# Kernel tuning notes

Measured on AMD Instinct MI355X. Metric: run time of the kernel, lower is better.

The kernel has to match this reference:

```python
import jax, jax.numpy as jnp
import numpy as np

N_MODEL = 32          # self.n_model
TEMP = 0.05           # softmax temperature
LARGE_NEG = -float(np.log(1e10))


def setup_inputs() -> dict:
    key = jax.random.key(0)
    ks = jax.random.split(key, 20)
    B, D, N, seq_len, d_model, pred_len, in_dim = 4, 32, 768, 96, 128, 24, 3
    L = 2 * seq_len
    w = lambda k, shape: jax.random.normal(k, shape, jnp.float32) * 0.02
    return {
        "x_t": jax.random.normal(ks[0], (B, N, 16), jnp.float32),   # unused by forward
        "x": jax.random.normal(ks[1], (B, D, N, L), jnp.float32),
        "csta": jax.random.uniform(ks[2], (N, 2), jnp.float32),
        "cpan": jax.random.uniform(ks[3], (B, N, 2), jnp.float32),
        # Time_Attention Q/K/V: Linear(2*seq_len, d_model)
        "Wq": w(ks[4], (d_model, L)), "bq": jnp.zeros((d_model,), jnp.float32),
        "Wk": w(ks[5], (d_model, L)), "bk": jnp.zeros((d_model,), jnp.float32),
        "Wv": w(ks[6], (d_model, L)), "bv": jnp.zeros((d_model,), jnp.float32),
        # geo-graph embeddings
        "W_sta": w(ks[7], (N_MODEL, 2)), "b_sta": jnp.zeros((N_MODEL,), jnp.float32),
        "W_n1": w(ks[8], (N_MODEL, 3 * N_MODEL)), "b_n1": jnp.zeros((N_MODEL,), jnp.float32),
        "W_n2": w(ks[9], (N_MODEL, 3 * N_MODEL)), "b_n2": jnp.zeros((N_MODEL,), jnp.float32),
        "distance_scale": jnp.asarray(2.0, jnp.float32),
        # output heads: fc1 Linear(d_model, pred_len), fc2 Linear(2*d_mark=32, in_dim)
        "W_fc1": w(ks[10], (pred_len, d_model)), "b_fc1": jnp.zeros((pred_len,), jnp.float32),
        "W_fc2": w(ks[11], (in_dim, 2 * 16)), "b_fc2": jnp.zeros((in_dim,), jnp.float32),
    }


def _l2norm(v, axis=1, eps=1e-12):
    n = jnp.sqrt(jnp.sum(v * v, axis=axis, keepdims=True))
    return v / jnp.maximum(n, eps)


def _geo_graph(csta_n, W_sta, b_sta, W_n1, b_n1, W_n2, b_n2, distance_scale):
    nodevec = csta_n @ W_sta.T + b_sta                      # [N, 32]
    node_c = jnp.concatenate([jnp.sin(nodevec), jnp.cos(nodevec), nodevec], axis=1)  # [N, 96]
    nv1 = _l2norm(jax.nn.relu(node_c @ W_n1.T + b_n1))
    nv2 = _l2norm(jax.nn.relu(node_c @ W_n2.T + b_n2))
    geo_sim = nv1 @ nv2.T                                   # [N, N]
    lat, lon = csta_n[:, 0], csta_n[:, 1]
    dist = jnp.sqrt((lat[:, None] - lat[None, :]) ** 2 + (lon[:, None] - lon[None, :]) ** 2 + 1e-8)
    dscale = jax.nn.sigmoid(distance_scale) * 3.0
    dist_sim = jnp.exp(-dist * dscale)
    combined = geo_sim * 0.6 + dist_sim * 0.4 + 0.05
    return (combined + combined.T) / 2.0


def reference(x_t, x, csta, cpan, Wq, bq, Wk, bk, Wv, bv,
              W_sta, b_sta, W_n1, b_n1, W_n2, b_n2, distance_scale,
              W_fc1, b_fc1, W_fc2, b_fc2):
    B, D, N, L = x.shape
    pred_len, d_model = W_fc1.shape
    in_dim = W_fc2.shape[0]

    # robust min-max normalization of station coordinates
    lat_v, lon_v = cpan[:, :, 0], cpan[:, :, 1]
    rng = jnp.stack([lat_v.max() - lat_v.min() + 1e-8, lon_v.max() - lon_v.min() + 1e-8])
    mins = jnp.stack([lat_v.min(), lon_v.min()])
    csta_n = (csta - mins) / rng                            # [N, 2]

    geo_graph = _geo_graph(csta_n, W_sta, b_sta, W_n1, b_n1, W_n2, b_n2, distance_scale)

    # Time_Attention over fused batch-channel axis
    xr = x.reshape(B * D, N, L)
    q = xr @ Wq.T + bq                                      # [BD, N, d]
    k = xr @ Wk.T + bk
    v = xr @ Wv.T + bv
    scale = 1.0 / np.sqrt(d_model)
    scores = jnp.einsum('bnd,bmd->bnm', q, k) * scale       # [BD, N, N]
    add_mask = jnp.where(geo_graph == 0, LARGE_NEG, 0.0)
    scores = scores * geo_graph[None] + add_mask[None]
    A = jax.nn.softmax(scores / TEMP, axis=-1)              # dropout = identity (eval)
    t = jnp.einsum('bnm,bmd->bnd', A, v)                    # [BD, N, d]

    out = t @ W_fc1.T + b_fc1                               # [BD, N, pred_len]
    out = out.reshape(B, D, N, pred_len).transpose(0, 3, 2, 1).reshape(-1, N, D)
    out = out @ W_fc2.T + b_fc2                             # [B*P, N, in_dim]
    out = out.reshape(B, pred_len, N, in_dim).transpose(0, 3, 2, 1)  # [B, in_dim, N, pred_len]
    return out, A, geo_graph
```

## Files before the change

kernel.cpp:

```cpp
#include <hip/hip_runtime.h>
#include <math.h>

#define NN 768
#define DM 128
#define LL 192
#define BD 128
#define OUT_OFF_A   221184
#define OUT_OFF_GEO 75718656

#define WS_CN   16
#define WS_NV1  2048
#define WS_NV2  26624
#define WS_GEOS 51200
#define WS_WH   641024
#define WS_W1H  677888
#define WS_QH   739328
#define WS_KH   7030784
#define WS_VT   13322240
#define WS_O1   19613696

constexpr float TEMP_INV    = 20.0f;
constexpr float QK_SCALE    = 0.08838834764831845f;
constexpr float LOG2E       = 1.4426950408889634f;
constexpr float GS_SCALE    = QK_SCALE * TEMP_INV * LOG2E;

typedef unsigned short u16;
typedef u16 u16x8 __attribute__((ext_vector_type(8)));
typedef u16 u16x4 __attribute__((ext_vector_type(4)));
typedef __bf16 bf16x8 __attribute__((ext_vector_type(8)));
typedef float f32x4 __attribute__((ext_vector_type(4)));

__device__ __forceinline__ u16 f2b(float f) {
  unsigned u = __builtin_bit_cast(unsigned, f);
  return (u16)((u + 0x7fffu + ((u >> 16) & 1u)) >> 16);
}

__device__ __forceinline__ void lds_barrier() {
  asm volatile("s_waitcnt lgkmcnt(0)" ::: "memory");
  __builtin_amdgcn_s_barrier();
}

__global__ __launch_bounds__(256) void k_prep(const float* __restrict__ cpan,
                                              const float* __restrict__ csta,
                                              float* __restrict__ ws) {
  __shared__ float red[4][4];
  int t = threadIdx.x;
  float mnla = 1e30f, mxla = -1e30f, mnlo = 1e30f, mxlo = -1e30f;
  for (int i = t; i < 3072; i += 256) {
    float la = cpan[i * 2 + 0], lo = cpan[i * 2 + 1];
    mnla = fminf(mnla, la); mxla = fmaxf(mxla, la);
    mnlo = fminf(mnlo, lo); mxlo = fmaxf(mxlo, lo);
  }
  for (int off = 1; off < 64; off <<= 1) {
    mnla = fminf(mnla, __shfl_xor(mnla, off));
    mxla = fmaxf(mxla, __shfl_xor(mxla, off));
    mnlo = fminf(mnlo, __shfl_xor(mnlo, off));
    mxlo = fmaxf(mxlo, __shfl_xor(mxlo, off));
  }
  if ((t & 63) == 0) {
    int w = t >> 6;
    red[0][w] = mnla; red[1][w] = mxla; red[2][w] = mnlo; red[3][w] = mxlo;
  }
  __syncthreads();
  mnla = fminf(fminf(red[0][0], red[0][1]), fminf(red[0][2], red[0][3]));
  mxla = fmaxf(fmaxf(red[1][0], red[1][1]), fmaxf(red[1][2], red[1][3]));
  mnlo = fminf(fminf(red[2][0], red[2][1]), fminf(red[2][2], red[2][3]));
  mxlo = fmaxf(fmaxf(red[3][0], red[3][1]), fmaxf(red[3][2], red[3][3]));
  float rla = mxla - mnla + 1e-8f;
  float rlo = mxlo - mnlo + 1e-8f;
  float* cn = ws + WS_CN;
  for (int i = t; i < NN; i += 256) {
    cn[i * 2 + 0] = (csta[i * 2 + 0] - mnla) / rla;
    cn[i * 2 + 1] = (csta[i * 2 + 1] - mnlo) / rlo;
  }
}

__global__ __launch_bounds__(256) void k_cvtw(const float* __restrict__ Wq, const float* __restrict__ Wk,
                                              const float* __restrict__ Wv, const float* __restrict__ W_fc1,
                                              u16* __restrict__ wh, u16* __restrict__ w1h) {
  int i = (blockIdx.x * 256 + threadIdx.x) * 4;
  if (i < 73728) {
    const float* src = (i < 24576) ? (Wq + i) : ((i < 49152) ? (Wk + i - 24576) : (Wv + i - 49152));
    float4 v = *(const float4*)src;
    u16x4 o = {f2b(v.x), f2b(v.y), f2b(v.z), f2b(v.w)};
    *(u16x4*)(wh + i) = o;
  } else {
    int j = i - 73728;
    if (j < 4096) {
      int row = j >> 7;
      u16x4 o = {0, 0, 0, 0};
      if (row < 24) {
        float4 v = *(const float4*)(W_fc1 + (size_t)row * 128 + (j & 127));
        o.x = f2b(v.x); o.y = f2b(v.y); o.z = f2b(v.z); o.w = f2b(v.w);
      }
      *(u16x4*)(w1h + j) = o;
    }
  }
}

__global__ __launch_bounds__(64) void k_nodes(const float* __restrict__ cn,
                                              const float* __restrict__ W_sta, const float* __restrict__ b_sta,
                                              const float* __restrict__ W_n1, const float* __restrict__ b_n1,
                                              const float* __restrict__ W_n2, const float* __restrict__ b_n2,
                                              float* __restrict__ nv1, float* __restrict__ nv2) {
  __shared__ float node_c[96];
  int i = blockIdx.x, t = threadIdx.x;
  float c0 = cn[i * 2 + 0], c1 = cn[i * 2 + 1];
  if (t < 32) {
    float nv = c0 * W_sta[t * 2 + 0] + c1 * W_sta[t * 2 + 1] + b_sta[t];
    node_c[t] = sinf(nv);
    node_c[32 + t] = cosf(nv);
    node_c[64 + t] = nv;
  }
  __syncthreads();
  int half = t >> 5, o = t & 31;
  const float* W = half ? W_n2 : W_n1;
  const float* b = half ? b_n2 : b_n1;
  float acc = b[o];
  for (int j = 0; j < 96; ++j) acc = fmaf(node_c[j], W[o * 96 + j], acc);
  acc = fmaxf(acc, 0.0f);
  float ss = acc * acc;
  for (int off = 1; off < 32; off <<= 1) ss += __shfl_xor(ss, off);
  float nrm = fmaxf(sqrtf(ss), 1e-12f);
  (half ? nv2 : nv1)[i * 32 + o] = acc / nrm;
}

__global__ __launch_bounds__(256) void k_geo(const float* __restrict__ nv1, const float* __restrict__ nv2,
                                             const float* __restrict__ cn, const float* __restrict__ dsc_in,
                                             float* __restrict__ geo, float* __restrict__ geoS) {
  int idx = blockIdx.x * 256 + threadIdx.x;
  if (idx >= NN * NN) return;
  int i = idx / NN, j = idx % NN;
  float d1 = 0.f, d2 = 0.f;
  for (int o = 0; o < 32; ++o) {
    d1 = fmaf(nv1[i * 32 + o], nv2[j * 32 + o], d1);
    d2 = fmaf(nv1[j * 32 + o], nv2[i * 32 + o], d2);
  }
  float dla = cn[i * 2] - cn[j * 2], dlo = cn[i * 2 + 1] - cn[j * 2 + 1];
  float dist = sqrtf(dla * dla + dlo * dlo + 1e-8f);
  float x = dsc_in[0];
  float dscale = (1.0f / (1.0f + expf(-x))) * 3.0f;
  float dsim = expf(-dist * dscale);
  float g = 0.3f * (d1 + d2) + 0.4f * dsim + 0.05f;
  geo[idx] = g;
  geoS[idx] = g * GS_SCALE;
}

__global__ __launch_bounds__(256) void k_qkv(const float* __restrict__ x, const u16* __restrict__ wh,
      const float* __restrict__ bq, const float* __restrict__ bk, const float* __restrict__ bv,
      u16* __restrict__ qo, u16* __restrict__ ko, u16* __restrict__ vTo) {
  int z = blockIdx.y;
  const u16* W = wh + z * 24576;
  const float* bias = (z == 0) ? bq : ((z == 1) ? bk : bv);
  __shared__ u16 xs[128 * 192];
  int m0 = blockIdx.x * 128;
  int t = threadIdx.x;
  const float* xg = x + (size_t)m0 * 192;
  for (int i = t; i < 3072; i += 256) {
    int row = i / 24, c = i % 24;
    float4 f0 = *(const float4*)(xg + (size_t)row * 192 + c * 8);
    float4 f1 = *(const float4*)(xg + (size_t)row * 192 + c * 8 + 4);
    u16x8 v8 = {f2b(f0.x), f2b(f0.y), f2b(f0.z), f2b(f0.w),
                f2b(f1.x), f2b(f1.y), f2b(f1.z), f2b(f1.w)};
    int byte = (row * 384 + c * 16) ^ ((row & 7) << 4);
    *(u16x8*)((char*)xs + byte) = v8;
  }
  __syncthreads();
  int w = t >> 6, l = t & 63, wr = w >> 1, wc = w & 1, lg = l >> 4, lm = l & 15;
  f32x4 acc[4][4] = {};
#pragma unroll
  for (int kk = 0; kk < 6; ++kk) {
    bf16x8 a[4], b[4];
#pragma unroll
    for (int fr = 0; fr < 4; ++fr) {
      int row = wr * 64 + fr * 16 + lm;
      int byte = (row * 384 + kk * 64 + lg * 16) ^ ((row & 7) << 4);
      a[fr] = __builtin_bit_cast(bf16x8, *(const u16x8*)((const char*)xs + byte));
    }
#pragma unroll
    for (int fc = 0; fc < 4; ++fc) {
      int row = wc * 64 + fc * 16 + lm;
      b[fc] = __builtin_bit_cast(bf16x8, *(const u16x8*)(W + row * 192 + kk * 32 + lg * 8));
    }
#pragma unroll
    for (int fr = 0; fr < 4; ++fr)
#pragma unroll
      for (int fc = 0; fc < 4; ++fc)
        acc[fr][fc] = __builtin_amdgcn_mfma_f32_16x16x32_bf16(a[fr], b[fc], acc[fr][fc], 0, 0, 0);
  }
  if (z < 2) {
    u16* out = (z == 0) ? qo : ko;
#pragma unroll
    for (int fr = 0; fr < 4; ++fr)
#pragma unroll
      for (int fc = 0; fc < 4; ++fc) {
        int col = wc * 64 + fc * 16 + lm;
        float bb = bias[col];
#pragma unroll
        for (int r = 0; r < 4; ++r) {
          int row = m0 + wr * 64 + fr * 16 + lg * 4 + r;
          out[(size_t)row * 128 + col] = f2b(acc[fr][fc][r] + bb);
        }
      }
  } else {
    u16* es = xs;
    __syncthreads();
#pragma unroll
    for (int fr = 0; fr < 4; ++fr)
#pragma unroll
      for (int fc = 0; fc < 4; ++fc) {
        int col = wc * 64 + fc * 16 + lm;
        float bb = bias[col];
#pragma unroll
        for (int r = 0; r < 4; ++r) {
          int row = wr * 64 + fr * 16 + lg * 4 + r;
          es[row * 132 + col] = f2b(acc[fr][fc][r] + bb);
        }
      }
    __syncthreads();
    int col = t >> 1, half = t & 1;
    int bd = m0 / NN, ml = m0 % NN;
    u16* dst = vTo + (size_t)bd * 98304 + (size_t)col * NN + ml + half * 64;
#pragma unroll
    for (int i = 0; i < 64; i += 8) {
      u16x8 v8;
#pragma unroll
      for (int j = 0; j < 8; ++j) v8[j] = es[(half * 64 + i + j) * 132 + col];
      *(u16x8*)(dst + i) = v8;
    }
  }
}

__global__ __launch_bounds__(256, 4) void k_attn(const u16* __restrict__ qh, const u16* __restrict__ kh,
                                                 const u16* __restrict__ vT, const float* __restrict__ geoS,
                                                 const u16* __restrict__ w1h, const float* __restrict__ b_fc1,
                                                 float* __restrict__ Aout, float* __restrict__ o1) {
  int bd = blockIdx.x;
  int m0 = blockIdx.y * 64;
  __shared__ u16 ks[2][32 * 128];
  __shared__ u16 vs[2][128 * 32];
  __shared__ u16 pb[4][16 * 32];
  int t = threadIdx.x, w = t >> 6, l = t & 63, lm = l & 15, hi = l >> 4;
  const u16* qg = qh + ((size_t)bd * NN + m0) * 128;
  const u16* kg = kh + (size_t)bd * 98304;
  const u16* vg = vT + (size_t)bd * 98304;
  float* Ab = Aout + (size_t)bd * 589824 + (size_t)m0 * NN;
  const float* gb = geoS + (size_t)m0 * NN;

  bf16x8 qf[4];
#pragma unroll
  for (int kk = 0; kk < 4; ++kk)
    qf[kk] = __builtin_bit_cast(bf16x8,
        *(const u16x8*)(qg + (size_t)(w * 16 + lm) * 128 + kk * 32 + hi * 8));

#pragma unroll
  for (int i = 0; i < 2; ++i) {
    int idx = i * 256 + t, row = idx >> 4, cc = idx & 15;
    u16x8 v8 = *(const u16x8*)(kg + (size_t)row * 128 + cc * 8);
    int byte = (row * 256 + cc * 16) ^ ((row & 7) << 4);
    *(u16x8*)((char*)ks[0] + byte) = v8;
  }
  float gcur[2][4];
#pragma unroll
  for (int fc = 0; fc < 2; ++fc)
#pragma unroll
    for (int r = 0; r < 4; ++r)
      gcur[fc][r] = gb[(size_t)(w * 16 + hi * 4 + r) * NN + fc * 16 + lm];
  lds_barrier();
  float psum[4] = {0.f, 0.f, 0.f, 0.f};
  for (int c = 0; c < 24; ++c) {
    u16x8 kpre[2];
    float gnxt[2][4];
    if (c < 23) {
#pragma unroll
      for (int i = 0; i < 2; ++i) {
        int idx = i * 256 + t, row = idx >> 4, cc = idx & 15;
        kpre[i] = *(const u16x8*)(kg + (size_t)((c + 1) * 32 + row) * 128 + cc * 8);
      }
#pragma unroll
      for (int fc = 0; fc < 2; ++fc)
#pragma unroll
        for (int r = 0; r < 4; ++r)
          gnxt[fc][r] = gb[(size_t)(w * 16 + hi * 4 + r) * NN + (c + 1) * 32 + fc * 16 + lm];
    }
    const u16* kb = ks[c & 1];
    f32x4 acc[2] = {};
#pragma unroll
    for (int kk = 0; kk < 4; ++kk)
#pragma unroll
      for (int fc = 0; fc < 2; ++fc) {
        int row = fc * 16 + lm;
        int byte = (row * 256 + kk * 64 + hi * 16) ^ ((row & 7) << 4);
        bf16x8 b = __builtin_bit_cast(bf16x8, *(const u16x8*)((const char*)kb + byte));
        acc[fc] = __builtin_amdgcn_mfma_f32_16x16x32_bf16(qf[kk], b, acc[fc], 0, 0, 0);
      }
    if (c < 23) {
#pragma unroll
      for (int i = 0; i < 2; ++i) {
        int idx = i * 256 + t, row = idx >> 4, cc = idx & 15;
        int byte = (row * 256 + cc * 16) ^ ((row & 7) << 4);
        *(u16x8*)((char*)ks[(c + 1) & 1] + byte) = kpre[i];
      }
    }
#pragma unroll
    for (int fc = 0; fc < 2; ++fc)
#pragma unroll
      for (int r = 0; r < 4; ++r)
        psum[r] += __builtin_amdgcn_exp2f(fminf(acc[fc][r] * gcur[fc][r], 120.0f));
    if (c < 23) {
#pragma unroll
      for (int fc = 0; fc < 2; ++fc)
#pragma unroll
        for (int r = 0; r < 4; ++r) gcur[fc][r] = gnxt[fc][r];
    }
    lds_barrier();
  }
#pragma unroll
  for (int off = 1; off < 16; off <<= 1)
#pragma unroll
    for (int r = 0; r < 4; ++r) psum[r] += __shfl_xor(psum[r], off);
  float inv[4];
#pragma unroll
  for (int r = 0; r < 4; ++r) inv[r] = 1.0f / psum[r];

#pragma unroll
  for (int i = 0; i < 2; ++i) {
    int idx = i * 256 + t;
    int krow = idx >> 4, kcc = idx & 15;
    u16x8 kv8 = *(const u16x8*)(kg + (size_t)krow * 128 + kcc * 8);
    int kbyte = (krow * 256 + kcc * 16) ^ ((krow & 7) << 4);
    *(u16x8*)((char*)ks[0] + kbyte) = kv8;
    int vrow = idx >> 2, vcc = idx & 3;
    u16x8 vv8 = *(const u16x8*)(vg + (size_t)vrow * NN + vcc * 8);
    int vbyte = (vrow * 64 + vcc * 16) ^ ((vrow & 7) << 4);
    *(u16x8*)((char*)vs[0] + vbyte) = vv8;
  }
#pragma unroll
  for (int fc = 0; fc < 2; ++fc)
#pragma unroll
    for (int r = 0; r < 4; ++r)
      gcur[fc][r] = gb[(size_t)(w * 16 + hi * 4 + r) * NN + fc * 16 + lm];
  lds_barrier();
  f32x4 tacc[8] = {};
  u16* pw = pb[w];
  for (int c = 0; c < 24; ++c) {
    u16x8 kpre[2], vpre[2];
    float gnxt[2][4];
    if (c < 23) {
#pragma unroll
      for (int i = 0; i < 2; ++i) {
        int idx = i * 256 + t;
        int krow = idx >> 4, kcc = idx & 15;
        kpre[i] = *(const u16x8*)(kg + (size_t)((c + 1) * 32 + krow) * 128 + kcc * 8);
        int vrow = idx >> 2, vcc = idx & 3;
        vpre[i] = *(const u16x8*)(vg + (size_t)vrow * NN + (c + 1) * 32 + vcc * 8);
      }
#pragma unroll
      for (int fc = 0; fc < 2; ++fc)
#pragma unroll
        for (int r = 0; r < 4; ++r)
          gnxt[fc][r] = gb[(size_t)(w * 16 + hi * 4 + r) * NN + (c + 1) * 32 + fc * 16 + lm];
    }
    const u16* kb = ks[c & 1];
    f32x4 acc[2] = {};
#pragma unroll
    for (int kk = 0; kk < 4; ++kk)
#pragma unroll
      for (int fc = 0; fc < 2; ++fc) {
        int row = fc * 16 + lm;
        int byte = (row * 256 + kk * 64 + hi * 16) ^ ((row & 7) << 4);
        bf16x8 b = __builtin_bit_cast(bf16x8, *(const u16x8*)((const char*)kb + byte));
        acc[fc] = __builtin_amdgcn_mfma_f32_16x16x32_bf16(qf[kk], b, acc[fc], 0, 0, 0);
      }
    if (c < 23) {
#pragma unroll
      for (int i = 0; i < 2; ++i) {
        int idx = i * 256 + t;
        int krow = idx >> 4, kcc = idx & 15;
        int kbyte = (krow * 256 + kcc * 16) ^ ((krow & 7) << 4);
        *(u16x8*)((char*)ks[(c + 1) & 1] + kbyte) = kpre[i];
        int vrow = idx >> 2, vcc = idx & 3;
        int vbyte = (vrow * 64 + vcc * 16) ^ ((vrow & 7) << 4);
        *(u16x8*)((char*)vs[(c + 1) & 1] + vbyte) = vpre[i];
      }
    }
#pragma unroll
    for (int fc = 0; fc < 2; ++fc) {
      int col = c * 32 + fc * 16 + lm;
#pragma unroll
      for (int r = 0; r < 4; ++r) {
        int rl = w * 16 + hi * 4 + r;
        float u = __builtin_amdgcn_exp2f(fminf(acc[fc][r] * gcur[fc][r], 120.0f));
        float p = u * inv[r];
        __builtin_nontemporal_store(p, Ab + (size_t)rl * NN + col);
        int rloc = hi * 4 + r;
        int byte = (rloc * 64 + (fc * 16 + lm) * 2) ^ ((rloc & 7) << 4);
        *(u16*)((char*)pw + byte) = f2b(p);
      }
    }
    if (c < 23) {
#pragma unroll
      for (int fc = 0; fc < 2; ++fc)
#pragma unroll
        for (int r = 0; r < 4; ++r) gcur[fc][r] = gnxt[fc][r];
    }
    bf16x8 pa;
    {
      int byte = (lm * 64 + hi * 16) ^ ((lm & 7) << 4);
      pa = __builtin_bit_cast(bf16x8, *(const u16x8*)((const char*)pw + byte));
    }
    const u16* vb = vs[c & 1];
#pragma unroll
    for (int fc = 0; fc < 8; ++fc) {
      int row = fc * 16 + lm;
      int byte = (row * 64 + hi * 16) ^ ((row & 7) << 4);
      bf16x8 b = __builtin_bit_cast(bf16x8, *(const u16x8*)((const char*)vb + byte));
      tacc[fc] = __builtin_amdgcn_mfma_f32_16x16x32_bf16(pa, b, tacc[fc], 0, 0, 0);
    }
    lds_barrier();
  }

  u16* ts = (u16*)ks + w * 2048;
#pragma unroll
  for (int fc = 0; fc < 8; ++fc)
#pragma unroll
    for (int r = 0; r < 4; ++r) {
      int row = hi * 4 + r, col = fc * 16 + lm;
      int byte = (row * 256 + col * 2) ^ ((row & 7) << 4);
      *(u16*)((char*)ts + byte) = f2b(tacc[fc][r]);
    }
  f32x4 of[2] = {};
#pragma unroll
  for (int kk = 0; kk < 4; ++kk) {
    int byte = (lm * 256 + kk * 64 + hi * 16) ^ ((lm & 7) << 4);
    bf16x8 tf = __builtin_bit_cast(bf16x8, *(const u16x8*)((const char*)ts + byte));
#pragma unroll
    for (int g = 0; g < 2; ++g) {
      bf16x8 wf = __builtin_bit_cast(bf16x8,
          *(const u16x8*)(w1h + (size_t)(g * 16 + lm) * 128 + kk * 32 + hi * 8));
      of[g] = __builtin_amdgcn_mfma_f32_16x16x32_bf16(tf, wf, of[g], 0, 0, 0);
    }
  }
  int bi = bd >> 5, di = bd & 31;
#pragma unroll
  for (int g = 0; g < 2; ++g) {
    int pp = g * 16 + lm;
    if (pp < 24) {
      float bb = b_fc1[pp];
#pragma unroll
      for (int r = 0; r < 4; ++r) {
        int n = m0 + w * 16 + hi * 4 + r;
        __builtin_nontemporal_store(of[g][r] + bb,
            o1 + ((size_t)(bi * NN + n) * 32 + di) * 24 + pp);
      }
    }
  }
}

__global__ __launch_bounds__(256) void k_final2(const float* __restrict__ o1, const float* __restrict__ W_fc2,
                                                const float* __restrict__ b_fc2, float* __restrict__ out) {
  __shared__ float ol[2][768];
  __shared__ float w2[96];
  int t = threadIdx.x, half = t >> 7, tl = t & 127;
  int b = blockIdx.x / 384, np = blockIdx.x % 384;
  int n = np * 2 + half;
  const float* src = o1 + (size_t)(b * NN + n) * 768;
  if (t < 96) w2[t] = W_fc2[t];
  for (int i = tl; i < 192; i += 128)
    *(float4*)&ol[half][i * 4] = *(const float4*)(src + i * 4);
  __syncthreads();
  if (tl < 72) {
    int c = tl / 24, pp = tl % 24;
    float acc = b_fc2[c];
#pragma unroll
    for (int d = 0; d < 32; ++d) acc = fmaf(w2[c * 32 + d], ol[half][d * 24 + pp], acc);
    out[(((size_t)b * 3 + c) * NN + n) * 24 + pp] = acc;
  }
}

extern "C" void kernel_launch(void* const* d_in, const int* in_sizes, int n_in,
                              void* d_out, int out_size, void* d_ws, size_t ws_size,
                              hipStream_t stream) {
  (void)in_sizes; (void)n_in; (void)out_size; (void)ws_size;
  const float* x     = (const float*)d_in[1];
  const float* csta  = (const float*)d_in[2];
  const float* cpan  = (const float*)d_in[3];
  const float* Wq    = (const float*)d_in[4];
  const float* bq    = (const float*)d_in[5];
  const float* Wk    = (const float*)d_in[6];
  const float* bk    = (const float*)d_in[7];
  const float* Wv    = (const float*)d_in[8];
  const float* bv    = (const float*)d_in[9];
  const float* W_sta = (const float*)d_in[10];
  const float* b_sta = (const float*)d_in[11];
  const float* W_n1  = (const float*)d_in[12];
  const float* b_n1  = (const float*)d_in[13];
  const float* W_n2  = (const float*)d_in[14];
  const float* b_n2  = (const float*)d_in[15];
  const float* dsc   = (const float*)d_in[16];
  const float* W_fc1 = (const float*)d_in[17];
  const float* b_fc1 = (const float*)d_in[18];
  const float* W_fc2 = (const float*)d_in[19];
  const float* b_fc2 = (const float*)d_in[20];

  float* out  = (float*)d_out;
  float* Aout = out + OUT_OFF_A;
  float* geo  = out + OUT_OFF_GEO;

  float* ws   = (float*)d_ws;
  float* cn   = ws + WS_CN;
  float* nv1  = ws + WS_NV1;
  float* nv2  = ws + WS_NV2;
  float* geoS = ws + WS_GEOS;
  u16*   wh   = (u16*)(ws + WS_WH);
  u16*   w1h  = (u16*)(ws + WS_W1H);
  u16*   qh   = (u16*)(ws + WS_QH);
  u16*   kh   = (u16*)(ws + WS_KH);
  u16*   vT   = (u16*)(ws + WS_VT);
  float* o1   = ws + WS_O1;

  k_prep<<<1, 256, 0, stream>>>(cpan, csta, ws);
  k_cvtw<<<76, 256, 0, stream>>>(Wq, Wk, Wv, W_fc1, wh, w1h);
  k_nodes<<<768, 64, 0, stream>>>(cn, W_sta, b_sta, W_n1, b_n1, W_n2, b_n2, nv1, nv2);
  k_geo<<<(NN * NN + 255) / 256, 256, 0, stream>>>(nv1, nv2, cn, dsc, geo, geoS);

  k_qkv<<<dim3(768, 3), 256, 0, stream>>>(x, wh, bq, bk, bv, qh, kh, vT);
  k_attn<<<dim3(BD, 12), 256, 0, stream>>>(qh, kh, vT, geoS, w1h, b_fc1, Aout, o1);
  k_final2<<<1536, 256, 0, stream>>>(o1, W_fc2, b_fc2, out);
}
```

Before: 269.8 us.

## Fuse QKV projections per block and widen attention pass-one K tiles

The QKV kernel now stages each x tile into shared memory once and computes all three projections (Q, K, V) in a single block, rather than launching three blocks per tile that each reload and convert x. In the attention kernel, the first softmax-normalisation pass now processes 64-key chunks over 12 iterations instead of 32-key chunks over 24, using a unified shared buffer that is re-partitioned for the second pass. This cuts redundant x reads and conversions and halves the barrier count in pass one, at the cost of fewer QKV blocks for parallelism and more registers for the larger accumulators and prefetch arrays.

After: 280.4 us. 3.9% more time.

```diff
diff --git a/kernel.cpp b/kernel.cpp
--- a/kernel.cpp
+++ b/kernel.cpp
@@ -149,9 +149,6 @@
 __global__ __launch_bounds__(256) void k_qkv(const float* __restrict__ x, const u16* __restrict__ wh,
       const float* __restrict__ bq, const float* __restrict__ bk, const float* __restrict__ bv,
       u16* __restrict__ qo, u16* __restrict__ ko, u16* __restrict__ vTo) {
-  int z = blockIdx.y;
-  const u16* W = wh + z * 24576;
-  const float* bias = (z == 0) ? bq : ((z == 1) ? bk : bv);
   __shared__ u16 xs[128 * 192];
   int m0 = blockIdx.x * 128;
   int t = threadIdx.x;
@@ -167,29 +164,35 @@
   }
   __syncthreads();
   int w = t >> 6, l = t & 63, wr = w >> 1, wc = w & 1, lg = l >> 4, lm = l & 15;
-  f32x4 acc[4][4] = {};
-#pragma unroll
-  for (int kk = 0; kk < 6; ++kk) {
-    bf16x8 a[4], b[4];
-#pragma unroll
-    for (int fr = 0; fr < 4; ++fr) {
-      int row = wr * 64 + fr * 16 + lm;
-      int byte = (row * 384 + kk * 64 + lg * 16) ^ ((row & 7) << 4);
-      a[fr] = __builtin_bit_cast(bf16x8, *(const u16x8*)((const char*)xs + byte));
-    }
-#pragma unroll
-    for (int fc = 0; fc < 4; ++fc) {
-      int row = wc * 64 + fc * 16 + lm;
-      b[fc] = __builtin_bit_cast(bf16x8, *(const u16x8*)(W + row * 192 + kk * 32 + lg * 8));
-    }
-#pragma unroll
-    for (int fr = 0; fr < 4; ++fr)
-#pragma unroll
-      for (int fc = 0; fc < 4; ++fc)
-        acc[fr][fc] = __builtin_amdgcn_mfma_f32_16x16x32_bf16(a[fr], b[fc], acc[fr][fc], 0, 0, 0);
-  }
-  if (z < 2) {
-    u16* out = (z == 0) ? qo : ko;
+
+  auto compute = [&](const u16* W, f32x4 (&acc)[4][4]) {
+#pragma unroll
+    for (int kk = 0; kk < 6; ++kk) {
+      bf16x8 a[4], b[4];
+#pragma unroll
+      for (int fr = 0; fr < 4; ++fr) {
+        int row = wr * 64 + fr * 16 + lm;
+        int byte = (row * 384 + kk * 64 + lg * 16) ^ ((row & 7) << 4);
+        a[fr] = __builtin_bit_cast(bf16x8, *(const u16x8*)((const char*)xs + byte));
+      }
+#pragma unroll
+      for (int fc = 0; fc < 4; ++fc) {
+        int row = wc * 64 + fc * 16 + lm;
+        b[fc] = __builtin_bit_cast(bf16x8, *(const u16x8*)(W + row * 192 + kk * 32 + lg * 8));
+      }
+#pragma unroll
+      for (int fr = 0; fr < 4; ++fr)
+#pragma unroll
+        for (int fc = 0; fc < 4; ++fc)
+          acc[fr][fc] = __builtin_amdgcn_mfma_f32_16x16x32_bf16(a[fr], b[fc], acc[fr][fc], 0, 0, 0);
+    }
+  };
+
+  for (int z = 0; z < 2; ++z) {
+    f32x4 acc[4][4] = {};
+    compute(wh + z * 24576, acc);
+    const float* bias = z == 0 ? bq : bk;
+    u16* out = z == 0 ? qo : ko;
 #pragma unroll
     for (int fr = 0; fr < 4; ++fr)
 #pragma unroll
@@ -202,7 +205,10 @@
           out[(size_t)row * 128 + col] = f2b(acc[fr][fc][r] + bb);
         }
       }
-  } else {
+  }
+  {
+    f32x4 acc[4][4] = {};
+    compute(wh + 2 * 24576, acc);
     u16* es = xs;
     __syncthreads();
 #pragma unroll
@@ -210,7 +216,7 @@
 #pragma unroll
       for (int fc = 0; fc < 4; ++fc) {
         int col = wc * 64 + fc * 16 + lm;
-        float bb = bias[col];
+        float bb = bv[col];
 #pragma unroll
         for (int r = 0; r < 4; ++r) {
           int row = wr * 64 + fr * 16 + lg * 4 + r;
@@ -237,8 +243,7 @@
                                                  float* __restrict__ Aout, float* __restrict__ o1) {
   int bd = blockIdx.x;
   int m0 = blockIdx.y * 64;
-  __shared__ u16 ks[2][32 * 128];
-  __shared__ u16 vs[2][128 * 32];
+  __shared__ u16 smem[16384];
   __shared__ u16 pb[4][16 * 32];
   int t = threadIdx.x, w = t >> 6, l = t & 63, lm = l & 15, hi = l >> 4;
   const u16* qg = qh + ((size_t)bd * NN + m0) * 128;
@@ -254,62 +259,63 @@
         *(const u16x8*)(qg + (size_t)(w * 16 + lm) * 128 + kk * 32 + hi * 8));
 
 #pragma unroll
-  for (int i = 0; i < 2; ++i) {
+  for (int i = 0; i < 4; ++i) {
     int idx = i * 256 + t, row = idx >> 4, cc = idx & 15;
     u16x8 v8 = *(const u16x8*)(kg + (size_t)row * 128 + cc * 8);
     int byte = (row * 256 + cc * 16) ^ ((row & 7) << 4);
-    *(u16x8*)((char*)ks[0] + byte) = v8;
-  }
-  float gcur[2][4];
-#pragma unroll
-  for (int fc = 0; fc < 2; ++fc)
+    *(u16x8*)((char*)smem + byte) = v8;
+  }
+  float gcur[4][4];
+#pragma unroll
+  for (int fc = 0; fc < 4; ++fc)
 #pragma unroll
     for (int r = 0; r < 4; ++r)
       gcur[fc][r] = gb[(size_t)(w * 16 + hi * 4 + r) * NN + fc * 16 + lm];
   lds_barrier();
   float psum[4] = {0.f, 0.f, 0.f, 0.f};
-  for (int c = 0; c < 24; ++c) {
-    u16x8 kpre[2];
-    float gnxt[2][4];
-    if (c < 23) {
-#pragma unroll
-      for (int i = 0; i < 2; ++i) {
+  for (int c = 0; c < 12; ++c) {
+    int cbuf = (c & 1) * 16384;
+    int nbuf = 16384 - cbuf;
+    u16x8 kpre[4];
+    float gnxt[4][4];
+    if (c < 11) {
+#pragma unroll
+      for (int i = 0; i < 4; ++i) {
         int idx = i * 256 + t, row = idx >> 4, cc = idx & 15;
-        kpre[i] = *(const u16x8*)(kg + (size_t)((c + 1) * 32 + row) * 128 + cc * 8);
-      }
-#pragma unroll
-      for (int fc = 0; fc < 2; ++fc)
+        kpre[i] = *(const u16x8*)(kg + (size_t)((c + 1) * 64 + row) * 128 + cc * 8);
+      }
+#pragma unroll
+      for (int fc = 0; fc < 4; ++fc)
 #pragma unroll
         for (int r = 0; r < 4; ++r)
-          gnxt[fc][r] = gb[(size_t)(w * 16 + hi * 4 + r) * NN + (c + 1) * 32 + fc * 16 + lm];
-    }
-    const u16* kb = ks[c & 1];
-    f32x4 acc[2] = {};
+          gnxt[fc][r] = gb[(size_t)(w * 16 + hi * 4 + r) * NN + (c + 1) * 64 + fc * 16 + lm];
+    }
+    f32x4 acc[4] = {};
 #pragma unroll
     for (int kk = 0; kk < 4; ++kk)
 #pragma unroll
-      for (int fc = 0; fc < 2; ++fc) {
+      for (int fc = 0; fc < 4; ++fc) {
         int row = fc * 16 + lm;
-        int byte = (row * 256 + kk * 64 + hi * 16) ^ ((row & 7) << 4);
-        bf16x8 b = __builtin_bit_cast(bf16x8, *(const u16x8*)((const char*)kb + byte));
+        int byte = cbuf + ((row * 256 + kk * 64 + hi * 16) ^ ((row & 7) << 4));
+        bf16x8 b = __builtin_bit_cast(bf16x8, *(const u16x8*)((const char*)smem + byte));
         acc[fc] = __builtin_amdgcn_mfma_f32_16x16x32_bf16(qf[kk], b, acc[fc], 0, 0, 0);
       }
-    if (c < 23) {
-#pragma unroll
-      for (int i = 0; i < 2; ++i) {
+    if (c < 11) {
+#pragma unroll
+      for (int i = 0; i < 4; ++i) {
         int idx = i * 256 + t, row = idx >> 4, cc = idx & 15;
-        int byte = (row * 256 + cc * 16) ^ ((row & 7) << 4);
-        *(u16x8*)((char*)ks[(c + 1) & 1] + byte) = kpre[i];
-      }
-    }
-#pragma unroll
-    for (int fc = 0; fc < 2; ++fc)
+        int byte = nbuf + ((row * 256 + cc * 16) ^ ((row & 7) << 4));
+        *(u16x8*)((char*)smem + byte) = kpre[i];
+      }
+    }
+#pragma unroll
+    for (int fc = 0; fc < 4; ++fc)
 #pragma unroll
       for (int r = 0; r < 4; ++r)
         psum[r] += __builtin_amdgcn_exp2f(fminf(acc[fc][r] * gcur[fc][r], 120.0f));
-    if (c < 23) {
-#pragma unroll
-      for (int fc = 0; fc < 2; ++fc)
+    if (c < 11) {
+#pragma unroll
+      for (int fc = 0; fc < 4; ++fc)
 #pragma unroll
         for (int r = 0; r < 4; ++r) gcur[fc][r] = gnxt[fc][r];
     }
@@ -329,21 +335,26 @@
     int krow = idx >> 4, kcc = idx & 15;
     u16x8 kv8 = *(const u16x8*)(kg + (size_t)krow * 128 + kcc * 8);
     int kbyte = (krow * 256 + kcc * 16) ^ ((krow & 7) << 4);
-    *(u16x8*)((char*)ks[0] + kbyte) = kv8;
+    *(u16x8*)((char*)smem + kbyte) = kv8;
     int vrow = idx >> 2, vcc = idx & 3;
     u16x8 vv8 = *(const u16x8*)(vg + (size_t)vrow * NN + vcc * 8);
-    int vbyte = (vrow * 64 + vcc * 16) ^ ((vrow & 7) << 4);
-    *(u16x8*)((char*)vs[0] + vbyte) = vv8;
-  }
+    int vbyte = 16384 + ((vrow * 64 + vcc * 16) ^ ((vrow & 7) << 4));
+    *(u16x8*)((char*)smem + vbyte) = vv8;
+  }
+  float g2[2][4];
 #pragma unroll
   for (int fc = 0; fc < 2; ++fc)
 #pragma unroll
     for (int r = 0; r < 4; ++r)
-      gcur[fc][r] = gb[(size_t)(w * 16 + hi * 4 + r) * NN + fc * 16 + lm];
+      g2[fc][r] = gb[(size_t)(w * 16 + hi * 4 + r) * NN + fc * 16 + lm];
   lds_barrier();
   f32x4 tacc[8] = {};
   u16* pw = pb[w];
   for (int c = 0; c < 24; ++c) {
+    int kcur = (c & 1) * 8192;
+    int knxt = 8192 - kcur;
+    int vcur = 16384 + (c & 1) * 8192;
+    int vnxt = 16384 + (8192 - (vcur - 16384));
     u16x8 kpre[2], vpre[2];
     float gnxt[2][4];
     if (c < 23) {
@@ -361,15 +372,14 @@
         for (int r = 0; r < 4; ++r)
           gnxt[fc][r] = gb[(size_t)(w * 16 + hi * 4 + r) * NN + (c + 1) * 32 + fc * 16 + lm];
     }
-    const u16* kb = ks[c & 1];
     f32x4 acc[2] = {};
 #pragma unroll
     for (int kk = 0; kk < 4; ++kk)
 #pragma unroll
       for (int fc = 0; fc < 2; ++fc) {
         int row = fc * 16 + lm;
-        int byte = (row * 256 + kk * 64 + hi * 16) ^ ((row & 7) << 4);
-        bf16x8 b = __builtin_bit_cast(bf16x8, *(const u16x8*)((const char*)kb + byte));
+        int byte = kcur + ((row * 256 + kk * 64 + hi * 16) ^ ((row & 7) << 4));
+        bf16x8 b = __builtin_bit_cast(bf16x8, *(const u16x8*)((const char*)smem + byte));
         acc[fc] = __builtin_amdgcn_mfma_f32_16x16x32_bf16(qf[kk], b, acc[fc], 0, 0, 0);
       }
     if (c < 23) {
@@ -377,11 +387,11 @@
       for (int i = 0; i < 2; ++i) {
         int idx = i * 256 + t;
         int krow = idx >> 4, kcc = idx & 15;
-        int kbyte = (krow * 256 + kcc * 16) ^ ((krow & 7) << 4);
-        *(u16x8*)((char*)ks[(c + 1) & 1] + kbyte) = kpre[i];
+        int kbyte = knxt + ((krow * 256 + kcc * 16) ^ ((krow & 7) << 4));
+        *(u16x8*)((char*)smem + kbyte) = kpre[i];
         int vrow = idx >> 2, vcc = idx & 3;
-        int vbyte = (vrow * 64 + vcc * 16) ^ ((vrow & 7) << 4);
-        *(u16x8*)((char*)vs[(c + 1) & 1] + vbyte) = vpre[i];
+        int vbyte = vnxt + ((vrow * 64 + vcc * 16) ^ ((vrow & 7) << 4));
+        *(u16x8*)((char*)smem + vbyte) = vpre[i];
       }
     }
 #pragma unroll
@@ -390,7 +400,7 @@
 #pragma unroll
       for (int r = 0; r < 4; ++r) {
         int rl = w * 16 + hi * 4 + r;
-        float u = __builtin_amdgcn_exp2f(fminf(acc[fc][r] * gcur[fc][r], 120.0f));
+        float u = __builtin_amdgcn_exp2f(fminf(acc[fc][r] * g2[fc][r], 120.0f));
         float p = u * inv[r];
         __builtin_nontemporal_store(p, Ab + (size_t)rl * NN + col);
         int rloc = hi * 4 + r;
@@ -402,38 +412,37 @@
 #pragma unroll
       for (int fc = 0; fc < 2; ++fc)
 #pragma unroll
-        for (int r = 0; r < 4; ++r) gcur[fc][r] = gnxt[fc][r];
+        for (int r = 0; r < 4; ++r) g2[fc][r] = gnxt[fc][r];
     }
     bf16x8 pa;
     {
       int byte = (lm * 64 + hi * 16) ^ ((lm & 7) << 4);
       pa = __builtin_bit_cast(bf16x8, *(const u16x8*)((const char*)pw + byte));
     }
-    const u16* vb = vs[c & 1];
 #pragma unroll
     for (int fc = 0; fc < 8; ++fc) {
       int row = fc * 16 + lm;
-      int byte = (row * 64 + hi * 16) ^ ((row & 7) << 4);
-      bf16x8 b = __builtin_bit_cast(bf16x8, *(const u16x8*)((const char*)vb + byte));
+      int byte = vcur + ((row * 64 + hi * 16) ^ ((row & 7) << 4));
+      bf16x8 b = __builtin_bit_cast(bf16x8, *(const u16x8*)((const char*)smem + byte));
       tacc[fc] = __builtin_amdgcn_mfma_f32_16x16x32_bf16(pa, b, tacc[fc], 0, 0, 0);
     }
     lds_barrier();
   }
 
-  u16* ts = (u16*)ks + w * 2048;
+  char* ts = (char*)smem + w * 4096;
 #pragma unroll
   for (int fc = 0; fc < 8; ++fc)
 #pragma unroll
     for (int r = 0; r < 4; ++r) {
       int row = hi * 4 + r, col = fc * 16 + lm;
       int byte = (row * 256 + col * 2) ^ ((row & 7) << 4);
-      *(u16*)((char*)ts + byte) = f2b(tacc[fc][r]);
+      *(u16*)(ts + byte) = f2b(tacc[fc][r]);
     }
   f32x4 of[2] = {};
 #pragma unroll
   for (int kk = 0; kk < 4; ++kk) {
     int byte = (lm * 256 + kk * 64 + hi * 16) ^ ((lm & 7) << 4);
-    bf16x8 tf = __builtin_bit_cast(bf16x8, *(const u16x8*)((const char*)ts + byte));
+    bf16x8 tf = __builtin_bit_cast(bf16x8, *(const u16x8*)(ts + byte));
 #pragma unroll
     for (int g = 0; g < 2; ++g) {
       bf16x8 wf = __builtin_bit_cast(bf16x8,
@@ -524,7 +533,7 @@
   k_nodes<<<768, 64, 0, stream>>>(cn, W_sta, b_sta, W_n1, b_n1, W_n2, b_n2, nv1, nv2);
   k_geo<<<(NN * NN + 255) / 256, 256, 0, stream>>>(nv1, nv2, cn, dsc, geo, geoS);
 
-  k_qkv<<<dim3(768, 3), 256, 0, stream>>>(x, wh, bq, bk, bv, qh, kh, vT);
+  k_qkv<<<768, 256, 0, stream>>>(x, wh, bq, bk, bv, qh, kh, vT);
   k_attn<<<dim3(BD, 12), 256, 0, stream>>>(qh, kh, vT, geoS, w1h, b_fc1, Aout, o1);
   k_final2<<<1536, 256, 0, stream>>>(o1, W_fc2, b_fc2, out);
 }
```
